# Kernel tuning notes

Measured on AMD Instinct MI355X. Metric: run time of the kernel, lower is better.

The kernel has to match this reference:

```python
import jax, jax.numpy as jnp
import numpy as np

D_MODEL = 1024
NHEAD = 16
HEAD_DIM = D_MODEL // NHEAD
HID = int(D_MODEL * 4.0 * (2.0 / 3.0))  # 2730, matches int(d_model*mlp_ratio*2/3)
EPS = 1e-5


def setup_inputs() -> dict:
    key = jax.random.key(0)
    ks = jax.random.split(key, 12)
    s = lambda fi, fo: (2.0 / (fi + fo)) ** 0.5
    inp = {
        "x": jax.random.normal(ks[0], (2, 2048, D_MODEL), dtype=jnp.float32),
        "ln1_w": jnp.ones((D_MODEL,), jnp.float32),
        "ln1_b": jnp.zeros((D_MODEL,), jnp.float32),
        "wq": jax.random.normal(ks[1], (D_MODEL, D_MODEL), jnp.float32) * s(D_MODEL, D_MODEL),
        "wk": jax.random.normal(ks[2], (D_MODEL, D_MODEL), jnp.float32) * s(D_MODEL, D_MODEL),
        "wv": jax.random.normal(ks[3], (D_MODEL, D_MODEL), jnp.float32) * s(D_MODEL, D_MODEL),
        "wg": jax.random.normal(ks[4], (D_MODEL, D_MODEL), jnp.float32) * s(D_MODEL, D_MODEL),
        "wo": jax.random.normal(ks[5], (D_MODEL, D_MODEL), jnp.float32) * s(D_MODEL, D_MODEL),
        "ln2_w": jnp.ones((D_MODEL,), jnp.float32),
        "ln2_b": jnp.zeros((D_MODEL,), jnp.float32),
        "w_in": jax.random.normal(ks[6], (D_MODEL, 2 * HID), jnp.float32) * s(D_MODEL, 2 * HID),
        "b_in": jnp.zeros((2 * HID,), jnp.float32),
        "w_out": jax.random.normal(ks[7], (HID, D_MODEL), jnp.float32) * s(HID, D_MODEL),
        "b_out": jnp.zeros((D_MODEL,), jnp.float32),
    }
    return inp


def _layernorm(x, w, b):
    mu = jnp.mean(x, axis=-1, keepdims=True)
    var = jnp.var(x, axis=-1, keepdims=True)
    return (x - mu) * jax.lax.rsqrt(var + EPS) * w + b


def _decay_matrix(S):
    # gamma_h = 1 - 2^{-5-h}, RetNet multiscale decays
    gamma = 1.0 - jnp.exp2(-5.0 - jnp.arange(NHEAD, dtype=jnp.float32))  # [H]
    n = jnp.arange(S, dtype=jnp.float32)
    exp = n[:, None] - n[None, :]                     # [S, S]
    mask = exp >= 0
    d = gamma[:, None, None] ** jnp.where(mask, exp, 0.0)  # [H, S, S]
    return jnp.where(mask[None], d, 0.0)


def _msr(xn, wq, wk, wv, wg, wo):
    B, S, _ = xn.shape
    split = lambda t: t.reshape(B, S, NHEAD, HEAD_DIM).transpose(0, 2, 1, 3)  # bhsd
    q = split(xn @ wq) * (HEAD_DIM ** -0.5)
    k = split(xn @ wk)
    v = split(xn @ wv)
    Dm = _decay_matrix(S)                                   # [H, S, S]
    scores = jnp.einsum("bhsd,bhtd->bhst", q, k) * Dm[None]  # causal decayed retention
    out = jnp.einsum("bhst,bhtd->bhsd", scores, v)
    # per-head normalization (GroupNorm over head dim, no affine)
    mu = jnp.mean(out, axis=-1, keepdims=True)
    var = jnp.var(out, axis=-1, keepdims=True)
    out = (out - mu) * jax.lax.rsqrt(var + 1e-6)
    out = out.transpose(0, 2, 1, 3).reshape(B, S, D_MODEL)
    out = out * jax.nn.silu(xn @ wg)                        # swish gate
    return out @ wo


def _swiglu(x, w_in, b_in, w_out, b_out):
    ab = x @ w_in + b_in
    a, b = ab[..., :HID], ab[..., HID:]
    return (a * jax.nn.silu(b)) @ w_out + b_out


def reference(x, ln1_w, ln1_b, wq, wk, wv, wg, wo, ln2_w, ln2_b, w_in, b_in, w_out, b_out):
    h = _msr(_layernorm(x, ln1_w, ln1_b), wq, wk, wv, wg, wo)
    x = x + h  # dropout/drop_path identity at eval
    x = x + _swiglu(_layernorm(x, ln2_w, ln2_b), w_in, b_in, w_out, b_out)
    return x
```

## Files before the change

kernel.cpp:

```cpp
#include <hip/hip_runtime.h>
#include <math.h>

#define D_MODEL 1024
#define NHEAD   16
#define HDIM    64
#define HID     2730
#define HID_PAD 2816
#define SEQ     2048
#define BATCH   2
#define NTOK    (BATCH * SEQ)
#define QKG     3072

typedef __attribute__((ext_vector_type(8))) short bf16x8;
typedef __attribute__((ext_vector_type(4))) float f32x4;
typedef __attribute__((ext_vector_type(4))) short s16x4;

static __device__ inline short f2bf(float f)
{
    union { float f; unsigned int u; } c; c.f = f;
    unsigned int r = c.u + 0x7FFFu + ((c.u >> 16) & 1u);
    return (short)(r >> 16);
}
static __device__ inline float bf2f(short s)
{
    union { unsigned int u; float f; } c;
    c.u = ((unsigned int)(unsigned short)s) << 16;
    return c.f;
}

#define GLD16(gsrc, ldst) \
    __builtin_amdgcn_global_load_lds((const __attribute__((address_space(1))) void*)(gsrc), \
                                     (__attribute__((address_space(3))) void*)(ldst), 16, 0, 0)


__global__ void ln_kernel(const float* __restrict__ x,
                          const float* __restrict__ w,
                          const float* __restrict__ b,
                          short* __restrict__ out,
                          float eps)
{
    int row = blockIdx.x;
    int t = threadIdx.x;
    const float4* xr = (const float4*)(x + (size_t)row * D_MODEL);
    float4 v = xr[t];
    float s  = v.x + v.y + v.z + v.w;
    float sq = v.x * v.x + v.y * v.y + v.z * v.z + v.w * v.w;
#pragma unroll
    for (int off = 32; off > 0; off >>= 1) {
        s  += __shfl_xor(s, off);
        sq += __shfl_xor(sq, off);
    }
    __shared__ float ss[4], ssq[4];
    int wave = t >> 6;
    if ((t & 63) == 0) { ss[wave] = s; ssq[wave] = sq; }
    __syncthreads();
    s  = ss[0] + ss[1] + ss[2] + ss[3];
    sq = ssq[0] + ssq[1] + ssq[2] + ssq[3];
    float mu  = s * (1.0f / D_MODEL);
    float var = sq * (1.0f / D_MODEL) - mu * mu;
    float inv = rsqrtf(var + eps);
    float4 wv = ((const float4*)w)[t];
    float4 bv = ((const float4*)b)[t];
    s16x4 o;
    o.x = f2bf((v.x - mu) * inv * wv.x + bv.x);
    o.y = f2bf((v.y - mu) * inv * wv.y + bv.y);
    o.z = f2bf((v.z - mu) * inv * wv.z + bv.z);
    o.w = f2bf((v.w - mu) * inv * wv.w + bv.w);
    *(s16x4*)(out + (size_t)row * D_MODEL + 4 * t) = o;
}

struct TJob {
    const float* src;
    short* dst;
    int ldsrc, coloff, nvalid, kvalid, KPAD, NPAD;
};
struct TJobs { TJob j[8]; };

__global__ __launch_bounds__(256) void transpose_all(TJobs jobs)
{
    TJob jb = jobs.j[blockIdx.z];
    int k0 = blockIdx.x * 64, n0 = blockIdx.y * 64;
    if (k0 >= jb.KPAD || n0 >= jb.NPAD) return;
    __shared__ float tile[64][65];
    int t = threadIdx.x;
    {
        int kk = t >> 2, np = (t & 3) << 4;
        int k = k0 + kk;
        bool kok = k < jb.kvalid;
        const float* srow = jb.src + (size_t)k * jb.ldsrc + jb.coloff + n0 + np;
#pragma unroll
        for (int i = 0; i < 16; ++i) {
            int n = n0 + np + i;
            tile[kk][np + i] = (kok && n < jb.nvalid) ? srow[i] : 0.0f;
        }
    }
    __syncthreads();
    {
        int nn = t >> 2, kp = (t & 3) << 4;
        short* drow = jb.dst + (size_t)(n0 + nn) * jb.KPAD + k0 + kp;
#pragma unroll
        for (int v4 = 0; v4 < 4; ++v4) {
            s16x4 o;
            o.x = f2bf(tile[kp + v4 * 4 + 0][nn]);
            o.y = f2bf(tile[kp + v4 * 4 + 1][nn]);
            o.z = f2bf(tile[kp + v4 * 4 + 2][nn]);
            o.w = f2bf(tile[kp + v4 * 4 + 3][nn]);
            *(s16x4*)(drow + v4 * 4) = o;
        }
    }
}

template<int EPI>
static __device__ __forceinline__ void gemm_core(
        const short* __restrict__ A, int lda,
        const short* __restrict__ Bt,
        const float* __restrict__ bias,
        const float* __restrict__ R, int ldr,
        void* __restrict__ C, int ldc, int K, int bm, int bn,
        short (*As)[4096], short (*Bs)[4096])
{
    int t = threadIdx.x;
    int w = t >> 6;
    int lane = t & 63;
    int quad = lane >> 4;
    int l15  = lane & 15;
    int x7   = l15 & 7;

    int p0 = t >> 3;
    int u  = (t & 7) ^ (p0 & 7);
    int scol = (u & 3) << 3;
    const short* gA0 = A  + (size_t)(bm + p0 + ((u >> 2) << 6)) * lda + scol;
    const short* gA1 = gA0 + (size_t)32 * lda;
    const short* gB0 = Bt + (size_t)(bn + p0 + ((u >> 2) << 6)) * K + scol;
    const short* gB1 = gB0 + (size_t)32 * K;
    int wb = w << 9;

    int wr = (w >> 1) * 64;
    int wc = (w & 1) * 64;
    int aoff = l15 * 64 + (((((w >> 1) << 2) | quad) ^ x7) << 3);
    int boff = l15 * 64 + (((((w & 1) << 2) | quad) ^ x7) << 3);

    f32x4 acc[4][4];
#pragma unroll
    for (int i = 0; i < 4; ++i)
#pragma unroll
        for (int j = 0; j < 4; ++j) acc[i][j] = (f32x4){0.f, 0.f, 0.f, 0.f};

    GLD16(gA0, &As[0][wb]);
    GLD16(gA1, &As[0][2048 + wb]);
    GLD16(gB0, &Bs[0][wb]);
    GLD16(gB1, &Bs[0][2048 + wb]);

    for (int k0 = 0; k0 < K; k0 += 32) {
        int cur = (k0 >> 5) & 1;
        __syncthreads();
        int k1 = k0 + 32;
        if (k1 < K) {
            GLD16(gA0 + k1, &As[cur ^ 1][wb]);
            GLD16(gA1 + k1, &As[cur ^ 1][2048 + wb]);
            GLD16(gB0 + k1, &Bs[cur ^ 1][wb]);
            GLD16(gB1 + k1, &Bs[cur ^ 1][2048 + wb]);
        }
        bf16x8 af[4], bfr[4];
#pragma unroll
        for (int i = 0; i < 4; ++i)
            af[i] = *(const bf16x8*)(&As[cur][i * 1024 + aoff]);
#pragma unroll
        for (int j = 0; j < 4; ++j)
            bfr[j] = *(const bf16x8*)(&Bs[cur][j * 1024 + boff]);
#pragma unroll
        for (int i = 0; i < 4; ++i)
#pragma unroll
            for (int j = 0; j < 4; ++j)
                acc[i][j] = __builtin_amdgcn_mfma_f32_16x16x32_bf16(af[i], bfr[j], acc[i][j], 0, 0, 0);
    }

#pragma unroll
    for (int i = 0; i < 4; ++i) {
        int gr = bm + wr + i * 16 + quad * 4;
#pragma unroll
        for (int j = 0; j < 4; ++j) {
            int gc = bn + wc + j * 16 + l15;
#pragma unroll
            for (int r = 0; r < 4; ++r) {
                float val = acc[i][j][r];
                size_t idx = (size_t)(gr + r) * ldc + gc;
                if (EPI == 0) {
                    ((short*)C)[idx] = f2bf(val);
                } else if (EPI == 1) {
                    ((float*)C)[idx] = val + R[(size_t)(gr + r) * ldr + gc];
                } else {
                    ((float*)C)[idx] = val + bias[gc] + R[(size_t)(gr + r) * ldr + gc];
                }
            }
        }
    }
}

__global__ __launch_bounds__(256, 4) void proj_kernel(
        const short* __restrict__ xn,
        const short* __restrict__ qkgT,
        short* __restrict__ qkg,
        const short* __restrict__ wvT,
        short* __restrict__ vT)
{
    __shared__ short As[2][4096];
    __shared__ short Bs[2][4096];
    int id = blockIdx.x;
    if (id < 768) {
        int bm = (id & 31) * 128, bn = (id >> 5) * 128;
        gemm_core<0>(xn, D_MODEL, qkgT, nullptr, nullptr, 0, qkg, QKG, D_MODEL, bm, bn, As, Bs);
    } else {
        int i2 = id - 768;
        int bn = (i2 & 31) * 128, bm = (i2 >> 5) * 128;
        gemm_core<0>(wvT, D_MODEL, xn, nullptr, nullptr, 0, vT, NTOK, D_MODEL, bm, bn, As, Bs);
    }
}

template<int EPI>
__global__ __launch_bounds__(256, 4) void gemm_n64(
        const short* __restrict__ A, int lda,
        const short* __restrict__ Bt,
        const float* __restrict__ bias,
        const float* __restrict__ R, int ldr,
        void* __restrict__ C, int ldc, int K)
{
    __shared__ short As[2][4096];
    __shared__ short Bs[2][2048];
    int bm = blockIdx.x * 128;
    int bn = blockIdx.y * 64;
    int t = threadIdx.x;
    int w = t >> 6;
    int lane = t & 63;
    int quad = lane >> 4;
    int l15  = lane & 15;
    int x7   = l15 & 7;

    int p0 = t >> 3;
    int u  = (t & 7) ^ (p0 & 7);
    int scol = (u & 3) << 3;
    const short* gA0 = A  + (size_t)(bm + p0 + ((u >> 2) << 6)) * lda + scol;
    const short* gA1 = gA0 + (size_t)32 * lda;
    const short* gB0 = Bt + (size_t)(bn + p0 + ((u >> 2) << 5)) * K + scol;
    int wb = w << 9;

    int wr = (w >> 1) * 64;
    int wc = (w & 1) * 32;
    int aoff = l15 * 64 + (((((w >> 1) << 2) | quad) ^ x7) << 3);
    int boff = l15 * 64 + (((((w & 1) << 2) | quad) ^ x7) << 3);

    f32x4 acc[4][2];
#pragma unroll
    for (int i = 0; i < 4; ++i)
#pragma unroll
        for (int j = 0; j < 2; ++j) acc[i][j] = (f32x4){0.f, 0.f, 0.f, 0.f};

    GLD16(gA0, &As[0][wb]);
    GLD16(gA1, &As[0][2048 + wb]);
    GLD16(gB0, &Bs[0][wb]);

    for (int k0 = 0; k0 < K; k0 += 32) {
        int cur = (k0 >> 5) & 1;
        __syncthreads();
        int k1 = k0 + 32;
        if (k1 < K) {
            GLD16(gA0 + k1, &As[cur ^ 1][wb]);
            GLD16(gA1 + k1, &As[cur ^ 1][2048 + wb]);
            GLD16(gB0 + k1, &Bs[cur ^ 1][wb]);
        }
        bf16x8 af[4], bfr[2];
#pragma unroll
        for (int i = 0; i < 4; ++i)
            af[i] = *(const bf16x8*)(&As[cur][i * 1024 + aoff]);
#pragma unroll
        for (int j = 0; j < 2; ++j)
            bfr[j] = *(const bf16x8*)(&Bs[cur][j * 1024 + boff]);
#pragma unroll
        for (int i = 0; i < 4; ++i)
#pragma unroll
            for (int j = 0; j < 2; ++j)
                acc[i][j] = __builtin_amdgcn_mfma_f32_16x16x32_bf16(af[i], bfr[j], acc[i][j], 0, 0, 0);
    }

#pragma unroll
    for (int i = 0; i < 4; ++i) {
        int gr = bm + wr + i * 16 + quad * 4;
#pragma unroll
        for (int j = 0; j < 2; ++j) {
            int gc = bn + wc + j * 16 + l15;
#pragma unroll
            for (int r = 0; r < 4; ++r) {
                float val = acc[i][j][r];
                size_t idx = (size_t)(gr + r) * ldc + gc;
                if (EPI == 0) {
                    ((short*)C)[idx] = f2bf(val);
                } else if (EPI == 1) {
                    ((float*)C)[idx] = val + R[(size_t)(gr + r) * ldr + gc];
                } else {
                    ((float*)C)[idx] = val + bias[gc] + R[(size_t)(gr + r) * ldr + gc];
                }
            }
        }
    }
}

__global__ __launch_bounds__(256, 2) void mlp_fused(
        const short* __restrict__ A,
        const short* __restrict__ w_inT,
        const float* __restrict__ b_in,
        short* __restrict__ hm)
{
    __shared__ short As[2][8192];
    __shared__ short Bs[2][4096];
    const int K = D_MODEL;
    int bm = blockIdx.x * 256;
    int bn = blockIdx.y * 64;
    int t = threadIdx.x;
    int w = t >> 6;
    int lane = t & 63;
    int quad = lane >> 4;
    int l15  = lane & 15;
    int x7   = l15 & 7;

    int li3 = lane >> 3;
    int u   = (lane & 7) ^ li3;
    int hi  = u >> 2;
    int qk  = (u & 3) << 3;
    const short* gA = A + (size_t)(bm + hi * 128 + w * 32 + li3) * K + qk;
    int f = hi * 4 + w;
    const short* gB = w_inT + (size_t)(((f & 1) ? HID_PAD : 0) + bn
                                       + ((f >> 1) << 4) + li3) * K + qk;

    int abase = l15 * 64 + ((((w >> 1) << 2) | quad) ^ x7) * 8;
    int bbase = l15 * 64 + ((((w & 1) << 2) | quad) ^ x7) * 8;

    f32x4 acc[8][4];
#pragma unroll
    for (int i = 0; i < 8; ++i)
#pragma unroll
        for (int j = 0; j < 4; ++j) acc[i][j] = (f32x4){0.f, 0.f, 0.f, 0.f};

#pragma unroll
    for (int c = 0; c < 4; ++c)
        GLD16(gA + (size_t)c * 8 * K, &As[0][w * 2048 + c * 512]);
#pragma unroll
    for (int c = 0; c < 2; ++c)
        GLD16(gB + (size_t)c * 8 * K, &Bs[0][w * 1024 + c * 512]);

    for (int k0 = 0; k0 < K; k0 += 32) {
        int cur = (k0 >> 5) & 1;
        __syncthreads();
        int k1 = k0 + 32;
        if (k1 < K) {
#pragma unroll
            for (int c = 0; c < 4; ++c)
                GLD16(gA + (size_t)c * 8 * K + k1, &As[cur ^ 1][w * 2048 + c * 512]);
#pragma unroll
            for (int c = 0; c < 2; ++c)
                GLD16(gB + (size_t)c * 8 * K + k1, &Bs[cur ^ 1][w * 1024 + c * 512]);
        }
        bf16x8 af[8], bfr[4];
#pragma unroll
        for (int m = 0; m < 8; ++m)
            af[m] = *(const bf16x8*)(&As[cur][m * 1024 + abase]);
#pragma unroll
        for (int jf = 0; jf < 4; ++jf)
            bfr[jf] = *(const bf16x8*)(&Bs[cur][jf * 1024 + bbase]);
#pragma unroll
        for (int m = 0; m < 8; ++m)
#pragma unroll
            for (int jf = 0; jf < 4; ++jf)
                acc[m][jf] = __builtin_amdgcn_mfma_f32_16x16x32_bf16(af[m], bfr[jf], acc[m][jf], 0, 0, 0);
    }

#pragma unroll
    for (int m = 0; m < 8; ++m) {
        int gr = bm + (w >> 1) * 128 + m * 16 + quad * 4;
#pragma unroll
        for (int jj = 0; jj < 2; ++jj) {
            int gc = bn + (((w & 1) << 1) + jj) * 16 + l15;
            bool ok = gc < HID;
            float ba = ok ? b_in[gc] : 0.0f;
            float bb = ok ? b_in[HID + gc] : 0.0f;
#pragma unroll
            for (int r = 0; r < 4; ++r) {
                float a  = acc[m][2 * jj][r] + ba;
                float bv = acc[m][2 * jj + 1][r] + bb;
                float val = ok ? a * (bv / (1.0f + expf(-bv))) : 0.0f;
                hm[(size_t)(gr + r) * HID_PAD + gc] = f2bf(val);
            }
        }
    }
}

#define PSTR 72

__global__ __launch_bounds__(512) void retention_mfma(
        const short* __restrict__ qkg,
        const short* __restrict__ vT,
        short* __restrict__ rg)
{
    int i  = blockIdx.x;
    int xg = i & 15;
    int h  = (i >> 4) & 15;
    int b  = i >> 8;
    int qb = b ? xg : 15 - xg;

    __shared__ short ks[2][4096];
    __shared__ short vt[2][4096];
    __shared__ short ps[8][16 * PSTR];

    int tid  = threadIdx.x;
    int w    = tid >> 6;
    int lane = tid & 63;
    int quad = lane >> 4;
    int l15  = lane & 15;
    int x7   = l15 & 7;

    float log2g = log1pf(-exp2f(-5.0f - (float)h)) * 1.4426950408889634f;
    int hcol = h * HDIM;
    int s0 = qb * 128;
    size_t tok0 = (size_t)b * SEQ;

    int sch  = tid >> 8;
    int p0r  = (tid >> 3) & 31;
    int ur   = (tid & 7) ^ (p0r & 7);
    int srw  = p0r + ((ur >> 2) << 5);
    int sc8  = (ur & 3) << 3;
    const short* kbase  = qkg + (tok0 + srw) * QKG + 1024 + hcol + sch * 32 + sc8;
    const short* vtbase = vT + (size_t)(hcol + srw) * NTOK + tok0 + sch * 32 + sc8;
    int lb = tid << 3;

    const short* qrow = qkg + (tok0 + s0 + w * 16 + l15) * QKG + hcol;
    bf16x8 qa0 = *(const bf16x8*)(qrow + quad * 8);
    bf16x8 qa1 = *(const bf16x8*)(qrow + 32 + quad * 8);

    float colfac[4];
#pragma unroll
    for (int tile = 0; tile < 4; ++tile)
        colfac[tile] = exp2f(-(float)(tile * 16 + l15) * log2g) * 0.125f;

    f32x4 oacc[4];
#pragma unroll
    for (int k = 0; k < 4; ++k) oacc[k] = (f32x4){0.f, 0.f, 0.f, 0.f};

    int sbase = s0 + w * 16 + quad * 4;
    int tmax = 2 * qb + 1;

    GLD16(kbase, &ks[0][lb]);
    GLD16(vtbase, &vt[0][lb]);

    for (int tb = 0; tb <= tmax; ++tb) {
        int cur = tb & 1;
        __syncthreads();
        if (tb < tmax) {
            GLD16(kbase + (size_t)(tb + 1) * 64 * QKG, &ks[cur ^ 1][lb]);
            GLD16(vtbase + (tb + 1) * 64, &vt[cur ^ 1][lb]);
        }

        f32x4 sacc[4];
#pragma unroll
        for (int k = 0; k < 4; ++k) sacc[k] = (f32x4){0.f, 0.f, 0.f, 0.f};
#pragma unroll
        for (int tile = 0; tile < 4; ++tile) {
            int kaddr = ((tile & 1) * 16 + l15) * 64 +
                        (((((tile >> 1) << 2) | quad) ^ x7) << 3);
            bf16x8 kb0 = *(const bf16x8*)(&ks[cur][kaddr]);
            bf16x8 kb1 = *(const bf16x8*)(&ks[cur][2048 + kaddr]);
            sacc[tile] = __builtin_amdgcn_mfma_f32_16x16x32_bf16(qa0, kb0, sacc[tile], 0, 0, 0);
            sacc[tile] = __builtin_amdgcn_mfma_f32_16x16x32_bf16(qa1, kb1, sacc[tile], 0, 0, 0);
        }

        int fbi = sbase - tb * 64;
        float rf[4];
#pragma unroll
        for (int reg = 0; reg < 4; ++reg)
            rf[reg] = exp2f((float)(fbi + reg) * log2g);

        if (tb * 64 + 63 > s0 + w * 16) {
#pragma unroll
            for (int tile = 0; tile < 4; ++tile) {
                int tt = tile * 16 + l15;
#pragma unroll
                for (int reg = 0; reg < 4; ++reg) {
                    float p = (fbi + reg >= tt) ? sacc[tile][reg] * rf[reg] * colfac[tile] : 0.0f;
                    ps[w][(quad * 4 + reg) * PSTR + tile * 16 + l15] = f2bf(p);
                }
            }
        } else {
#pragma unroll
            for (int tile = 0; tile < 4; ++tile)
#pragma unroll
                for (int reg = 0; reg < 4; ++reg)
                    ps[w][(quad * 4 + reg) * PSTR + tile * 16 + l15] =
                        f2bf(sacc[tile][reg] * (rf[reg] * colfac[tile]));
        }

#pragma unroll
        for (int ksi = 0; ksi < 2; ++ksi) {
            bf16x8 pa = *(const bf16x8*)(&ps[w][l15 * PSTR + ksi * 32 + quad * 8]);
#pragma unroll
            for (int dt = 0; dt < 4; ++dt) {
                int vaddr = ((dt & 1) * 16 + l15) * 64 +
                            (((((dt >> 1) << 2) | quad) ^ x7) << 3);
                bf16x8 vb = *(const bf16x8*)(&vt[cur][ksi * 2048 + vaddr]);
                oacc[dt] = __builtin_amdgcn_mfma_f32_16x16x32_bf16(pa, vb, oacc[dt], 0, 0, 0);
            }
        }
    }

    float s1[4], s2[4];
#pragma unroll
    for (int reg = 0; reg < 4; ++reg) {
        s1[reg] = oacc[0][reg] + oacc[1][reg] + oacc[2][reg] + oacc[3][reg];
        s2[reg] = oacc[0][reg] * oacc[0][reg] + oacc[1][reg] * oacc[1][reg]
                + oacc[2][reg] * oacc[2][reg] + oacc[3][reg] * oacc[3][reg];
    }
#pragma unroll
    for (int off = 1; off < 16; off <<= 1) {
#pragma unroll
        for (int reg = 0; reg < 4; ++reg) {
            s1[reg] += __shfl_xor(s1[reg], off);
            s2[reg] += __shfl_xor(s2[reg], off);
        }
    }
    size_t rowtok = tok0 + s0 + w * 16 + quad * 4;
    short* obase = rg + rowtok * D_MODEL + hcol;
    const short* gbase = qkg + rowtok * QKG + 2048 + hcol;
#pragma unroll
    for (int reg = 0; reg < 4; ++reg) {
        float mu  = s1[reg] * (1.0f / 64.0f);
        float var = s2[reg] * (1.0f / 64.0f) - mu * mu;
        float inv = rsqrtf(var + 1e-6f);
#pragma unroll
        for (int dt = 0; dt < 4; ++dt) {
            float gv = bf2f(gbase[(size_t)reg * QKG + dt * 16 + l15]);
            float val = (oacc[dt][reg] - mu) * inv * (gv / (1.0f + expf(-gv)));
            obase[(size_t)reg * D_MODEL + dt * 16 + l15] = f2bf(val);
        }
    }
}

extern "C" void kernel_launch(void* const* d_in, const int* in_sizes, int n_in,
                              void* d_out, int out_size, void* d_ws, size_t ws_size,
                              hipStream_t stream)
{
    const float* x     = (const float*)d_in[0];
    const float* ln1w  = (const float*)d_in[1];
    const float* ln1b  = (const float*)d_in[2];
    const float* wq    = (const float*)d_in[3];
    const float* wk    = (const float*)d_in[4];
    const float* wv    = (const float*)d_in[5];
    const float* wg    = (const float*)d_in[6];
    const float* wo    = (const float*)d_in[7];
    const float* ln2w  = (const float*)d_in[8];
    const float* ln2b  = (const float*)d_in[9];
    const float* w_in  = (const float*)d_in[10];
    const float* b_in  = (const float*)d_in[11];
    const float* w_out = (const float*)d_in[12];
    const float* b_out = (const float*)d_in[13];
    float* out = (float*)d_out;
    char* base = (char*)d_ws;

    const size_t MB = 1u << 20;
    short* xn     = (short*)(base);
    short* qkgT   = (short*)(base +  8 * MB);
    short* wvT    = (short*)(base + 14 * MB);
    short* woT    = (short*)(base + 16 * MB);
    short* w_inT  = (short*)(base + 18 * MB);
    short* w_outT = (short*)(base + 29 * MB);
    short* qkg    = (short*)(base + 35 * MB);
    short* hm     = (short*)(base + 35 * MB);
    short* vT     = (short*)(base + 59 * MB);
    short* rg     = (short*)(base + 67 * MB);

    TJobs jobs;
    jobs.j[0] = { wq,    qkgT,                          1024,    0, 1024, 1024, 1024, 1024 };
    jobs.j[1] = { wk,    qkgT + 1024 * 1024,            1024,    0, 1024, 1024, 1024, 1024 };
    jobs.j[2] = { wg,    qkgT + 2 * 1024 * 1024,        1024,    0, 1024, 1024, 1024, 1024 };
    jobs.j[3] = { wv,    wvT,                           1024,    0, 1024, 1024, 1024, 1024 };
    jobs.j[4] = { wo,    woT,                           1024,    0, 1024, 1024, 1024, 1024 };
    jobs.j[5] = { w_in,  w_inT,                         2 * HID, 0,   HID, 1024, 1024, HID_PAD };
    jobs.j[6] = { w_in,  w_inT + (size_t)HID_PAD * 1024, 2 * HID, HID, HID, 1024, 1024, HID_PAD };
    jobs.j[7] = { w_out, w_outT,                        1024,    0, 1024, HID, HID_PAD, 1024 };
    transpose_all<<<dim3(44, 44, 8), 256, 0, stream>>>(jobs);

    ln_kernel<<<NTOK, 256, 0, stream>>>(x, ln1w, ln1b, xn, 1e-5f);
    proj_kernel<<<1024, 256, 0, stream>>>(xn, qkgT, qkg, wvT, vT);
    retention_mfma<<<512, 512, 0, stream>>>(qkg, vT, rg);
    gemm_n64<1><<<dim3(32, 16), 256, 0, stream>>>(rg, D_MODEL, woT, nullptr, x, D_MODEL, out, D_MODEL, D_MODEL);
    ln_kernel<<<NTOK, 256, 0, stream>>>(out, ln2w, ln2b, xn, 1e-5f);
    mlp_fused<<<dim3(NTOK / 256, HID_PAD / 64), 256, 0, stream>>>(xn, w_inT, b_in, hm);
    gemm_n64<2><<<dim3(32, 16), 256, 0, stream>>>(hm, HID_PAD, w_outT, b_out, out, D_MODEL, out, D_MODEL, HID_PAD);
}
```

Before: 398.5 us.

## Use 256x128 tiles for QKG/V projection and swap MLP grid order

Rewrites the projection kernel so each block computes a 256x128 tile with 8x4 MFMA fragments per wave, replacing the shared 128x128 gemm_core path. This halves the block count and increases operand reuse per LDS load, at the cost of more registers and lower occupancy (launch bounds 2). The MLP kernel's grid is also transposed so consecutive blocks walk along N over the same A rows, which changes L2 reuse of the activation tile.

```diff
diff --git a/kernel.cpp b/kernel.cpp
--- a/kernel.cpp
+++ b/kernel.cpp
@@ -110,15 +110,29 @@
     }
 }
 
-template<int EPI>
-static __device__ __forceinline__ void gemm_core(
-        const short* __restrict__ A, int lda,
-        const short* __restrict__ Bt,
-        const float* __restrict__ bias,
-        const float* __restrict__ R, int ldr,
-        void* __restrict__ C, int ldc, int K, int bm, int bn,
-        short (*As)[4096], short (*Bs)[4096])
-{
+__global__ __launch_bounds__(256, 2) void proj_kernel(
+        const short* __restrict__ xn,
+        const short* __restrict__ qkgT,
+        short* __restrict__ qkg,
+        const short* __restrict__ wvT,
+        short* __restrict__ vT)
+{
+    __shared__ short As[2][8192];
+    __shared__ short Bs[2][4096];
+    const int K = D_MODEL;
+    int id = blockIdx.x;
+    const short *A, *Bt;
+    short* C;
+    int ldc, bm, bn;
+    if (id < 384) {
+        A = xn; Bt = qkgT; C = qkg; ldc = QKG;
+        bm = (id & 15) * 256; bn = (id >> 4) * 128;
+    } else {
+        int i2 = id - 384;
+        A = wvT; Bt = xn; C = vT; ldc = NTOK;
+        bm = (i2 & 3) * 256; bn = (i2 >> 2) * 128;
+    }
+
     int t = threadIdx.x;
     int w = t >> 6;
     int lane = t & 63;
@@ -126,30 +140,109 @@
     int l15  = lane & 15;
     int x7   = l15 & 7;
 
+    int li3 = lane >> 3;
+    int u   = (lane & 7) ^ li3;
+    int hi  = u >> 2;
+    int qk  = (u & 3) << 3;
+    const short* gA = A + (size_t)(bm + hi * 128 + w * 32 + li3) * K + qk;
+    const short* gB = Bt + (size_t)(bn + hi * 64 + w * 16 + li3) * K + qk;
+
+    int abase = l15 * 64 + ((((w >> 1) << 2) | quad) ^ x7) * 8;
+    int bbase = l15 * 64 + ((((w & 1) << 2) | quad) ^ x7) * 8;
+
+    f32x4 acc[8][4];
+#pragma unroll
+    for (int i = 0; i < 8; ++i)
+#pragma unroll
+        for (int j = 0; j < 4; ++j) acc[i][j] = (f32x4){0.f, 0.f, 0.f, 0.f};
+
+#pragma unroll
+    for (int c = 0; c < 4; ++c)
+        GLD16(gA + (size_t)c * 8 * K, &As[0][w * 2048 + c * 512]);
+#pragma unroll
+    for (int c = 0; c < 2; ++c)
+        GLD16(gB + (size_t)c * 8 * K, &Bs[0][w * 1024 + c * 512]);
+
+    for (int k0 = 0; k0 < K; k0 += 32) {
+        int cur = (k0 >> 5) & 1;
+        __syncthreads();
+        int k1 = k0 + 32;
+        if (k1 < K) {
+#pragma unroll
+            for (int c = 0; c < 4; ++c)
+                GLD16(gA + (size_t)c * 8 * K + k1, &As[cur ^ 1][w * 2048 + c * 512]);
+#pragma unroll
+            for (int c = 0; c < 2; ++c)
+                GLD16(gB + (size_t)c * 8 * K + k1, &Bs[cur ^ 1][w * 1024 + c * 512]);
+        }
+        bf16x8 af[8], bfr[4];
+#pragma unroll
+        for (int m = 0; m < 8; ++m)
+            af[m] = *(const bf16x8*)(&As[cur][m * 1024 + abase]);
+#pragma unroll
+        for (int jf = 0; jf < 4; ++jf)
+            bfr[jf] = *(const bf16x8*)(&Bs[cur][jf * 1024 + bbase]);
+#pragma unroll
+        for (int m = 0; m < 8; ++m)
+#pragma unroll
+            for (int jf = 0; jf < 4; ++jf)
+                acc[m][jf] = __builtin_amdgcn_mfma_f32_16x16x32_bf16(af[m], bfr[jf], acc[m][jf], 0, 0, 0);
+    }
+
+#pragma unroll
+    for (int m = 0; m < 8; ++m) {
+        int gr = bm + (w >> 1) * 128 + m * 16 + quad * 4;
+#pragma unroll
+        for (int jf = 0; jf < 4; ++jf) {
+            int gc = bn + (w & 1) * 64 + jf * 16 + l15;
+#pragma unroll
+            for (int r = 0; r < 4; ++r)
+                C[(size_t)(gr + r) * ldc + gc] = f2bf(acc[m][jf][r]);
+        }
+    }
+}
+
+template<int EPI>
+__global__ __launch_bounds__(256, 4) void gemm_n64(
+        const short* __restrict__ A, int lda,
+        const short* __restrict__ Bt,
+        const float* __restrict__ bias,
+        const float* __restrict__ R, int ldr,
+        void* __restrict__ C, int ldc, int K)
+{
+    __shared__ short As[2][4096];
+    __shared__ short Bs[2][2048];
+    int bm = blockIdx.x * 128;
+    int bn = blockIdx.y * 64;
+    int t = threadIdx.x;
+    int w = t >> 6;
+    int lane = t & 63;
+    int quad = lane >> 4;
+    int l15  = lane & 15;
+    int x7   = l15 & 7;
+
     int p0 = t >> 3;
     int u  = (t & 7) ^ (p0 & 7);
     int scol = (u & 3) << 3;
     const short* gA0 = A  + (size_t)(bm + p0 + ((u >> 2) << 6)) * lda + scol;
     const short* gA1 = gA0 + (size_t)32 * lda;
-    const short* gB0 = Bt + (size_t)(bn + p0 + ((u >> 2) << 6)) * K + scol;
-    const short* gB1 = gB0 + (size_t)32 * K;
+    const short* gB0 = Bt + (size_t)(bn + p0 + ((u >> 2) << 5)) * K + scol;
     int wb = w << 9;
 
     int wr = (w >> 1) * 64;
-    int wc = (w & 1) * 64;
+    int wc = (w & 1) * 32;
     int aoff = l15 * 64 + (((((w >> 1) << 2) | quad) ^ x7) << 3);
     int boff = l15 * 64 + (((((w & 1) << 2) | quad) ^ x7) << 3);
 
-    f32x4 acc[4][4];
+    f32x4 acc[4][2];
 #pragma unroll
     for (int i = 0; i < 4; ++i)
 #pragma unroll
-        for (int j = 0; j < 4; ++j) acc[i][j] = (f32x4){0.f, 0.f, 0.f, 0.f};
+        for (int j = 0; j < 2; ++j) acc[i][j] = (f32x4){0.f, 0.f, 0.f, 0.f};
 
     GLD16(gA0, &As[0][wb]);
     GLD16(gA1, &As[0][2048 + wb]);
     GLD16(gB0, &Bs[0][wb]);
-    GLD16(gB1, &Bs[0][2048 + wb]);
 
     for (int k0 = 0; k0 < K; k0 += 32) {
         int cur = (k0 >> 5) & 1;
@@ -159,19 +252,18 @@
             GLD16(gA0 + k1, &As[cur ^ 1][wb]);
             GLD16(gA1 + k1, &As[cur ^ 1][2048 + wb]);
             GLD16(gB0 + k1, &Bs[cur ^ 1][wb]);
-            GLD16(gB1 + k1, &Bs[cur ^ 1][2048 + wb]);
-        }
-        bf16x8 af[4], bfr[4];
+        }
+        bf16x8 af[4], bfr[2];
 #pragma unroll
         for (int i = 0; i < 4; ++i)
             af[i] = *(const bf16x8*)(&As[cur][i * 1024 + aoff]);
 #pragma unroll
-        for (int j = 0; j < 4; ++j)
+        for (int j = 0; j < 2; ++j)
             bfr[j] = *(const bf16x8*)(&Bs[cur][j * 1024 + boff]);
 #pragma unroll
         for (int i = 0; i < 4; ++i)
 #pragma unroll
-            for (int j = 0; j < 4; ++j)
+            for (int j = 0; j < 2; ++j)
                 acc[i][j] = __builtin_amdgcn_mfma_f32_16x16x32_bf16(af[i], bfr[j], acc[i][j], 0, 0, 0);
     }
 
@@ -179,7 +271,7 @@
     for (int i = 0; i < 4; ++i) {
         int gr = bm + wr + i * 16 + quad * 4;
 #pragma unroll
-        for (int j = 0; j < 4; ++j) {
+        for (int j = 0; j < 2; ++j) {
             int gc = bn + wc + j * 16 + l15;
 #pragma unroll
             for (int r = 0; r < 4; ++r) {
@@ -197,113 +289,6 @@
     }
 }
 
-__global__ __launch_bounds__(256, 4) void proj_kernel(
-        const short* __restrict__ xn,
-        const short* __restrict__ qkgT,
-        short* __restrict__ qkg,
-        const short* __restrict__ wvT,
-        short* __restrict__ vT)
-{
-    __shared__ short As[2][4096];
-    __shared__ short Bs[2][4096];
-    int id = blockIdx.x;
-    if (id < 768) {
-        int bm = (id & 31) * 128, bn = (id >> 5) * 128;
-        gemm_core<0>(xn, D_MODEL, qkgT, nullptr, nullptr, 0, qkg, QKG, D_MODEL, bm, bn, As, Bs);
-    } else {
-        int i2 = id - 768;
-        int bn = (i2 & 31) * 128, bm = (i2 >> 5) * 128;
-        gemm_core<0>(wvT, D_MODEL, xn, nullptr, nullptr, 0, vT, NTOK, D_MODEL, bm, bn, As, Bs);
-    }
-}
-
-template<int EPI>
-__global__ __launch_bounds__(256, 4) void gemm_n64(
-        const short* __restrict__ A, int lda,
-        const short* __restrict__ Bt,
-        const float* __restrict__ bias,
-        const float* __restrict__ R, int ldr,
-        void* __restrict__ C, int ldc, int K)
-{
-    __shared__ short As[2][4096];
-    __shared__ short Bs[2][2048];
-    int bm = blockIdx.x * 128;
-    int bn = blockIdx.y * 64;
-    int t = threadIdx.x;
-    int w = t >> 6;
-    int lane = t & 63;
-    int quad = lane >> 4;
-    int l15  = lane & 15;
-    int x7   = l15 & 7;
-
-    int p0 = t >> 3;
-    int u  = (t & 7) ^ (p0 & 7);
-    int scol = (u & 3) << 3;
-    const short* gA0 = A  + (size_t)(bm + p0 + ((u >> 2) << 6)) * lda + scol;
-    const short* gA1 = gA0 + (size_t)32 * lda;
-    const short* gB0 = Bt + (size_t)(bn + p0 + ((u >> 2) << 5)) * K + scol;
-    int wb = w << 9;
-
-    int wr = (w >> 1) * 64;
-    int wc = (w & 1) * 32;
-    int aoff = l15 * 64 + (((((w >> 1) << 2) | quad) ^ x7) << 3);
-    int boff = l15 * 64 + (((((w & 1) << 2) | quad) ^ x7) << 3);
-
-    f32x4 acc[4][2];
-#pragma unroll
-    for (int i = 0; i < 4; ++i)
-#pragma unroll
-        for (int j = 0; j < 2; ++j) acc[i][j] = (f32x4){0.f, 0.f, 0.f, 0.f};
-
-    GLD16(gA0, &As[0][wb]);
-    GLD16(gA1, &As[0][2048 + wb]);
-    GLD16(gB0, &Bs[0][wb]);
-
-    for (int k0 = 0; k0 < K; k0 += 32) {
-        int cur = (k0 >> 5) & 1;
-        __syncthreads();
-        int k1 = k0 + 32;
-        if (k1 < K) {
-            GLD16(gA0 + k1, &As[cur ^ 1][wb]);
-            GLD16(gA1 + k1, &As[cur ^ 1][2048 + wb]);
-            GLD16(gB0 + k1, &Bs[cur ^ 1][wb]);
-        }
-        bf16x8 af[4], bfr[2];
-#pragma unroll
-        for (int i = 0; i < 4; ++i)
-            af[i] = *(const bf16x8*)(&As[cur][i * 1024 + aoff]);
-#pragma unroll
-        for (int j = 0; j < 2; ++j)
-            bfr[j] = *(const bf16x8*)(&Bs[cur][j * 1024 + boff]);
-#pragma unroll
-        for (int i = 0; i < 4; ++i)
-#pragma unroll
-            for (int j = 0; j < 2; ++j)
-                acc[i][j] = __builtin_amdgcn_mfma_f32_16x16x32_bf16(af[i], bfr[j], acc[i][j], 0, 0, 0);
-    }
-
-#pragma unroll
-    for (int i = 0; i < 4; ++i) {
-        int gr = bm + wr + i * 16 + quad * 4;
-#pragma unroll
-        for (int j = 0; j < 2; ++j) {
-            int gc = bn + wc + j * 16 + l15;
-#pragma unroll
-            for (int r = 0; r < 4; ++r) {
-                float val = acc[i][j][r];
-                size_t idx = (size_t)(gr + r) * ldc + gc;
-                if (EPI == 0) {
-                    ((short*)C)[idx] = f2bf(val);
-                } else if (EPI == 1) {
-                    ((float*)C)[idx] = val + R[(size_t)(gr + r) * ldr + gc];
-                } else {
-                    ((float*)C)[idx] = val + bias[gc] + R[(size_t)(gr + r) * ldr + gc];
-                }
-            }
-        }
-    }
-}
-
 __global__ __launch_bounds__(256, 2) void mlp_fused(
         const short* __restrict__ A,
         const short* __restrict__ w_inT,
@@ -313,8 +298,8 @@
     __shared__ short As[2][8192];
     __shared__ short Bs[2][4096];
     const int K = D_MODEL;
-    int bm = blockIdx.x * 256;
-    int bn = blockIdx.y * 64;
+    int bm = blockIdx.y * 256;
+    int bn = blockIdx.x * 64;
     int t = threadIdx.x;
     int w = t >> 6;
     int lane = t & 63;
@@ -586,10 +571,10 @@
     transpose_all<<<dim3(44, 44, 8), 256, 0, stream>>>(jobs);
 
     ln_kernel<<<NTOK, 256, 0, stream>>>(x, ln1w, ln1b, xn, 1e-5f);
-    proj_kernel<<<1024, 256, 0, stream>>>(xn, qkgT, qkg, wvT, vT);
+    proj_kernel<<<512, 256, 0, stream>>>(xn, qkgT, qkg, wvT, vT);
     retention_mfma<<<512, 512, 0, stream>>>(qkg, vT, rg);
     gemm_n64<1><<<dim3(32, 16), 256, 0, stream>>>(rg, D_MODEL, woT, nullptr, x, D_MODEL, out, D_MODEL, D_MODEL);
     ln_kernel<<<NTOK, 256, 0, stream>>>(out, ln2w, ln2b, xn, 1e-5f);
-    mlp_fused<<<dim3(NTOK / 256, HID_PAD / 64), 256, 0, stream>>>(xn, w_inT, b_in, hm);
+    mlp_fused<<<dim3(HID_PAD / 64, NTOK / 256), 256, 0, stream>>>(xn, w_inT, b_in, hm);
     gemm_n64<2><<<dim3(32, 16), 256, 0, stream>>>(hm, HID_PAD, w_outT, b_out, out, D_MODEL, out, D_MODEL, HID_PAD);
 }
```

Result: no change. 394.5 us (-1.0%).
